# Optimization experiments

Measured on AMD Instinct MI355X. Metric: run time of the kernel, lower is better.

Reference implementation:

```python
import jax, jax.numpy as jnp
import numpy as np

N_CLASSES = 2
N_FEATURES = 10
PSI_DIM = 10


def setup_inputs() -> dict:
    key = jax.random.key(0)
    k1, k2, k3, k4, k5 = jax.random.split(key, 5)
    T = 4_000_000
    x = jax.random.normal(k1, (T, N_FEATURES), dtype=jnp.float32)
    psi_real = jax.random.normal(k2, (PSI_DIM,), dtype=jnp.float32)
    psi_imag = jax.random.normal(k3, (PSI_DIM,), dtype=jnp.float32)
    A_real = jax.random.normal(k4, (N_CLASSES, PSI_DIM, PSI_DIM, N_FEATURES), dtype=jnp.float32)
    A_imag = jax.random.normal(k5, (N_CLASSES, PSI_DIM, PSI_DIM, N_FEATURES), dtype=jnp.float32)
    return {"x": x, "psi_real": psi_real, "psi_imag": psi_imag,
            "A_real": A_real, "A_imag": A_imag}


def _mat(psi1, A, psi2):
    # Batch-independent contraction of the 'i' and 'j' axes: [k, a]
    return jnp.einsum('i,kija,j->ka', psi1, A, psi2)


def reference(x, psi_real, psi_imag, A_real, A_imag):
    x_real = x
    x_imag = jnp.zeros_like(x)
    # Sign pattern from the original 8-term sum:
    #   +rRr -rIr(xi) -iRr(xi) -iIr(xr) -rRi(xr) +rIi(xi) +iRi(xi) +iIi(xr)
    # Coefficient matrix multiplying x_real:
    M_r = (_mat(psi_real, A_real, psi_real)
           - _mat(psi_imag, A_imag, psi_real)
           - _mat(psi_real, A_real, psi_imag)
           + _mat(psi_imag, A_imag, psi_imag))  # [k, a]
    # Coefficient matrix multiplying x_imag:
    M_i = (-_mat(psi_real, A_imag, psi_real)
           - _mat(psi_imag, A_real, psi_real)
           + _mat(psi_real, A_imag, psi_imag)
           + _mat(psi_imag, A_real, psi_imag))  # [k, a]
    # result[t, k] = sum_a x[t, a] * M[k, a]
    return x_real @ M_r.T + x_imag @ M_i.T
```

## Files before the change

### kernel.cpp

```cpp
#include <hip/hip_runtime.h>

constexpr int NC = 2;
constexpr int NF = 10;
constexpr int PD = 10;

__global__ void compute_M_kernel(const float* __restrict__ psi_r,
                                 const float* __restrict__ psi_i,
                                 const float* __restrict__ A_r,
                                 const float* __restrict__ A_i,
                                 float* __restrict__ M) {
    int t = threadIdx.x;
    if (t >= NC * NF) return;
    int k = t / NF;
    int a = t - k * NF;
    float acc = 0.f;
    for (int i = 0; i < PD; ++i) {
        float pri = psi_r[i];
        float pii = psi_i[i];
        for (int j = 0; j < PD; ++j) {
            float dj = psi_r[j] - psi_i[j];
            int idx = ((k * PD + i) * PD + j) * NF + a;
            acc = fmaf(pri * A_r[idx] - pii * A_i[idx], dj, acc);
        }
    }
    M[t] = acc;
}

__global__ __launch_bounds__(256) void apply_M_kernel(
        const float* __restrict__ x, const float* __restrict__ M,
        float* __restrict__ out, int T2) {
    float m0[NF], m1[NF];
#pragma unroll
    for (int a = 0; a < NF; ++a) {
        m0[a] = M[a];
        m1[a] = M[NF + a];
    }
    const int stride = gridDim.x * blockDim.x;
    for (int idx = blockIdx.x * blockDim.x + threadIdx.x; idx < T2; idx += stride) {
        const float4* xp = reinterpret_cast<const float4*>(x + (size_t)idx * 2 * NF);
        float4 v0 = xp[0];
        float4 v1 = xp[1];
        float4 v2 = xp[2];
        float4 v3 = xp[3];
        float4 v4 = xp[4];
        float r0[NF] = {v0.x, v0.y, v0.z, v0.w, v1.x, v1.y, v1.z, v1.w, v2.x, v2.y};
        float r1[NF] = {v2.z, v2.w, v3.x, v3.y, v3.z, v3.w, v4.x, v4.y, v4.z, v4.w};
        float4 o = {0.f, 0.f, 0.f, 0.f};
#pragma unroll
        for (int a = 0; a < NF; ++a) {
            o.x = fmaf(r0[a], m0[a], o.x);
            o.y = fmaf(r0[a], m1[a], o.y);
            o.z = fmaf(r1[a], m0[a], o.z);
            o.w = fmaf(r1[a], m1[a], o.w);
        }
        reinterpret_cast<float4*>(out)[idx] = o;
    }
}

extern "C" void kernel_launch(void* const* d_in, const int* in_sizes, int n_in,
                              void* d_out, int out_size, void* d_ws, size_t ws_size,
                              hipStream_t stream) {
    const float* x     = (const float*)d_in[0];
    const float* psi_r = (const float*)d_in[1];
    const float* psi_i = (const float*)d_in[2];
    const float* A_r   = (const float*)d_in[3];
    const float* A_i   = (const float*)d_in[4];
    float* out = (float*)d_out;
    float* M   = (float*)d_ws;

    const int T  = in_sizes[0] / NF;
    const int T2 = T / 2;

    compute_M_kernel<<<1, 64, 0, stream>>>(psi_r, psi_i, A_r, A_i, M);

    const int threads = 256;
    int blocks = (T2 + threads - 1) / threads;
    if (blocks > 2048) blocks = 2048;
    apply_M_kernel<<<blocks, threads, 0, stream>>>(x, M, out, T2);
}
```

Before: 39.95 us.

## Fuse M computation into apply kernel and stage x via direct global-to-LDS loads

Merges the single-block coefficient kernel into the main kernel, so every block recomputes the 20-entry M matrix in parallel (200 partial sums reduced in shared memory). This removes a kernel launch and the serial dependency between the two launches. The input rows are now loaded as coalesced float4 tiles straight into LDS with global_load_lds, and each thread reads its own 80 bytes back from LDS, instead of issuing strided 80-byte per-thread global loads. In exchange, every block repeats the M work and pays two barriers per tile, and the grid changes to 1792 blocks.

```diff
diff --git a/kernel.cpp b/kernel.cpp
--- a/kernel.cpp
+++ b/kernel.cpp
@@ -4,56 +4,93 @@
 constexpr int NF = 10;
 constexpr int PD = 10;
 
-__global__ void compute_M_kernel(const float* __restrict__ psi_r,
-                                 const float* __restrict__ psi_i,
-                                 const float* __restrict__ A_r,
-                                 const float* __restrict__ A_i,
-                                 float* __restrict__ M) {
-    int t = threadIdx.x;
-    if (t >= NC * NF) return;
-    int k = t / NF;
-    int a = t - k * NF;
-    float acc = 0.f;
-    for (int i = 0; i < PD; ++i) {
-        float pri = psi_r[i];
-        float pii = psi_i[i];
+constexpr int THREADS = 256;
+constexpr int F4_PER_THREAD = 5;
+constexpr int TILE_F4 = THREADS * F4_PER_THREAD;
+constexpr int TILE_FLOATS = TILE_F4 * 4;
+
+__global__ __launch_bounds__(THREADS) void fused_complexnet_kernel(
+        const float* __restrict__ x,
+        const float* __restrict__ psi_r,
+        const float* __restrict__ psi_i,
+        const float* __restrict__ A_r,
+        const float* __restrict__ A_i,
+        float* __restrict__ out,
+        int T2, long totalF4) {
+    __shared__ float Msh[NC * NF];
+    __shared__ float part[NC * NF * PD];
+    __shared__ float tile[TILE_FLOATS];
+
+    const int t = threadIdx.x;
+
+    if (t < NC * NF * PD) {
+        int k = t / (NF * PD);
+        int rem = t - k * (NF * PD);
+        int a = rem / PD;
+        int i = rem - a * PD;
+        float pri = psi_r[i], pii = psi_i[i];
+        float acc = 0.f;
+#pragma unroll
         for (int j = 0; j < PD; ++j) {
             float dj = psi_r[j] - psi_i[j];
             int idx = ((k * PD + i) * PD + j) * NF + a;
             acc = fmaf(pri * A_r[idx] - pii * A_i[idx], dj, acc);
         }
+        part[t] = acc;
     }
-    M[t] = acc;
-}
+    __syncthreads();
+    if (t < NC * NF) {
+        int k = t / NF, a = t - k * NF;
+        float s = 0.f;
+#pragma unroll
+        for (int i = 0; i < PD; ++i) s += part[(k * NF + a) * PD + i];
+        Msh[t] = s;
+    }
+    __syncthreads();
 
-__global__ __launch_bounds__(256) void apply_M_kernel(
-        const float* __restrict__ x, const float* __restrict__ M,
-        float* __restrict__ out, int T2) {
     float m0[NF], m1[NF];
 #pragma unroll
     for (int a = 0; a < NF; ++a) {
-        m0[a] = M[a];
-        m1[a] = M[NF + a];
+        m0[a] = Msh[a];
+        m1[a] = Msh[NF + a];
     }
-    const int stride = gridDim.x * blockDim.x;
-    for (int idx = blockIdx.x * blockDim.x + threadIdx.x; idx < T2; idx += stride) {
-        const float4* xp = reinterpret_cast<const float4*>(x + (size_t)idx * 2 * NF);
-        float4 v0 = xp[0];
-        float4 v1 = xp[1];
-        float4 v2 = xp[2];
-        float4 v3 = xp[3];
-        float4 v4 = xp[4];
-        float r0[NF] = {v0.x, v0.y, v0.z, v0.w, v1.x, v1.y, v1.z, v1.w, v2.x, v2.y};
-        float r1[NF] = {v2.z, v2.w, v3.x, v3.y, v3.z, v3.w, v4.x, v4.y, v4.z, v4.w};
-        float4 o = {0.f, 0.f, 0.f, 0.f};
+
+    const float4* x4 = reinterpret_cast<const float4*>(x);
+    float4* out4 = reinterpret_cast<float4*>(out);
+    const int nTiles = (T2 + THREADS - 1) / THREADS;
+    const int waveBaseF = (t & ~63) * 4;
+
+    for (int tileIdx = blockIdx.x; tileIdx < nTiles; tileIdx += (int)gridDim.x) {
+        const long base4 = (long)tileIdx * TILE_F4;
 #pragma unroll
-        for (int a = 0; a < NF; ++a) {
-            o.x = fmaf(r0[a], m0[a], o.x);
-            o.y = fmaf(r0[a], m1[a], o.y);
-            o.z = fmaf(r1[a], m0[a], o.z);
-            o.w = fmaf(r1[a], m1[a], o.w);
+        for (int q = 0; q < F4_PER_THREAD; ++q) {
+            long g4 = base4 + (long)q * THREADS + t;
+            if (g4 >= totalF4) g4 = totalF4 - 1;
+            const float* ldsdst = &tile[q * (THREADS * 4) + waveBaseF];
+            __builtin_amdgcn_global_load_lds(
+                (const __attribute__((address_space(1))) void*)(x4 + g4),
+                (__attribute__((address_space(3))) void*)ldsdst,
+                16, 0, 0);
         }
-        reinterpret_cast<float4*>(out)[idx] = o;
+        __syncthreads();
+
+        const int rp = tileIdx * THREADS + t;
+        if (rp < T2) {
+            const float4* lp = reinterpret_cast<const float4*>(&tile[t * 20]);
+            float4 v0 = lp[0], v1 = lp[1], v2 = lp[2], v3 = lp[3], v4 = lp[4];
+            float r0[NF] = {v0.x, v0.y, v0.z, v0.w, v1.x, v1.y, v1.z, v1.w, v2.x, v2.y};
+            float r1[NF] = {v2.z, v2.w, v3.x, v3.y, v3.z, v3.w, v4.x, v4.y, v4.z, v4.w};
+            float4 o = {0.f, 0.f, 0.f, 0.f};
+#pragma unroll
+            for (int a = 0; a < NF; ++a) {
+                o.x = fmaf(r0[a], m0[a], o.x);
+                o.y = fmaf(r0[a], m1[a], o.y);
+                o.z = fmaf(r1[a], m0[a], o.z);
+                o.w = fmaf(r1[a], m1[a], o.w);
+            }
+            out4[rp] = o;
+        }
+        __syncthreads();
     }
 }
 
@@ -66,15 +103,14 @@
     const float* A_r   = (const float*)d_in[3];
     const float* A_i   = (const float*)d_in[4];
     float* out = (float*)d_out;
-    float* M   = (float*)d_ws;
 
-    const int T  = in_sizes[0] / NF;
+    const int T = in_sizes[0] / NF;
     const int T2 = T / 2;
+    const long totalF4 = (long)in_sizes[0] / 4;
 
-    compute_M_kernel<<<1, 64, 0, stream>>>(psi_r, psi_i, A_r, A_i, M);
+    const int nTiles = (T2 + THREADS - 1) / THREADS;
+    int blocks = nTiles < 1792 ? nTiles : 1792;
 
-    const int threads = 256;
-    int blocks = (T2 + threads - 1) / threads;
-    if (blocks > 2048) blocks = 2048;
-    apply_M_kernel<<<blocks, threads, 0, stream>>>(x, M, out, T2);
+    fused_complexnet_kernel<<<blocks, THREADS, 0, stream>>>(
+        x, psi_r, psi_i, A_r, A_i, out, T2, totalF4);
 }
```

Measured after the change: 34.34 us. 1.16x faster.

## Fuse M computation into streaming kernel with double-buffered global-to-LDS loads

Applied to the files above, without the earlier changes.

Merges the two kernels into one: every wave recomputes the 2x10 coefficient matrix and broadcasts it with lane shuffles, removing the second launch and the workspace round trip. Each wave then streams 64-row tiles of x straight into LDS with direct global-to-LDS loads, double-buffered and ordered by hand-placed vmcnt waits, and writes a float2 per row. The cost is redundant per-wave recomputation of M, which reads A from global memory, plus reliance on exact vmcnt counting. Rows left over when T is not a multiple of 64 are not processed.

```diff
diff --git a/kernel.cpp b/kernel.cpp
--- a/kernel.cpp
+++ b/kernel.cpp
@@ -4,56 +4,95 @@
 constexpr int NF = 10;
 constexpr int PD = 10;
 
-__global__ void compute_M_kernel(const float* __restrict__ psi_r,
-                                 const float* __restrict__ psi_i,
-                                 const float* __restrict__ A_r,
-                                 const float* __restrict__ A_i,
-                                 float* __restrict__ M) {
-    int t = threadIdx.x;
-    if (t >= NC * NF) return;
-    int k = t / NF;
-    int a = t - k * NF;
+constexpr int THREADS = 256;
+constexpr int NWAVES = THREADS / 64;
+constexpr int TILE_ROWS = 64;
+constexpr int TILE_F4 = TILE_ROWS * NF / 4;
+constexpr int TILE_FLOATS = TILE_ROWS * NF;
+
+__global__ __launch_bounds__(THREADS, 8) void fused_stream_kernel(
+        const float* __restrict__ x,
+        const float* __restrict__ psi_r,
+        const float* __restrict__ psi_i,
+        const float* __restrict__ A_r,
+        const float* __restrict__ A_i,
+        float* __restrict__ out,
+        int nTiles) {
+    __shared__ float tile[NWAVES][2][TILE_FLOATS];
+
+    const int t = threadIdx.x;
+    const int w = t >> 6;
+    const int l = t & 63;
+
     float acc = 0.f;
-    for (int i = 0; i < PD; ++i) {
-        float pri = psi_r[i];
-        float pii = psi_i[i];
-        for (int j = 0; j < PD; ++j) {
-            float dj = psi_r[j] - psi_i[j];
-            int idx = ((k * PD + i) * PD + j) * NF + a;
-            acc = fmaf(pri * A_r[idx] - pii * A_i[idx], dj, acc);
+    if (l < NC * NF) {
+        const int kk = l / NF;
+        const int a = l - kk * NF;
+        for (int i = 0; i < PD; ++i) {
+            float pri = psi_r[i], pii = psi_i[i];
+#pragma unroll
+            for (int j = 0; j < PD; ++j) {
+                float dj = psi_r[j] - psi_i[j];
+                int idx = ((kk * PD + i) * PD + j) * NF + a;
+                acc = fmaf(pri * A_r[idx] - pii * A_i[idx], dj, acc);
+            }
         }
     }
-    M[t] = acc;
-}
-
-__global__ __launch_bounds__(256) void apply_M_kernel(
-        const float* __restrict__ x, const float* __restrict__ M,
-        float* __restrict__ out, int T2) {
     float m0[NF], m1[NF];
 #pragma unroll
     for (int a = 0; a < NF; ++a) {
-        m0[a] = M[a];
-        m1[a] = M[NF + a];
+        m0[a] = __shfl(acc, a);
+        m1[a] = __shfl(acc, NF + a);
     }
-    const int stride = gridDim.x * blockDim.x;
-    for (int idx = blockIdx.x * blockDim.x + threadIdx.x; idx < T2; idx += stride) {
-        const float4* xp = reinterpret_cast<const float4*>(x + (size_t)idx * 2 * NF);
-        float4 v0 = xp[0];
-        float4 v1 = xp[1];
-        float4 v2 = xp[2];
-        float4 v3 = xp[3];
-        float4 v4 = xp[4];
-        float r0[NF] = {v0.x, v0.y, v0.z, v0.w, v1.x, v1.y, v1.z, v1.w, v2.x, v2.y};
-        float r1[NF] = {v2.z, v2.w, v3.x, v3.y, v3.z, v3.w, v4.x, v4.y, v4.z, v4.w};
-        float4 o = {0.f, 0.f, 0.f, 0.f};
+
+    const float4* x4 = reinterpret_cast<const float4*>(x);
+    float2* out2 = reinterpret_cast<float2*>(out);
+    const int W = (int)gridDim.x * NWAVES;
+    const int gw = (int)blockIdx.x * NWAVES + w;
+
+    auto STAGE = [&](int buf, int tk) {
+        const float* dst = &tile[w][buf][0];
+        const float4* src = x4 + (long)tk * TILE_F4;
+        __builtin_amdgcn_global_load_lds(
+            (const __attribute__((address_space(1))) void*)(src + l),
+            (__attribute__((address_space(3))) void*)dst, 16, 0, 0);
+        __builtin_amdgcn_global_load_lds(
+            (const __attribute__((address_space(1))) void*)(src + 64 + l),
+            (__attribute__((address_space(3))) void*)(dst + 256), 16, 0, 0);
+        if (l < 32) {
+            __builtin_amdgcn_global_load_lds(
+                (const __attribute__((address_space(1))) void*)(src + 128 + l),
+                (__attribute__((address_space(3))) void*)(dst + 512), 16, 0, 0);
+        }
+    };
+
+    if (gw >= nTiles) return;
+
+    STAGE(0, gw);
+    int cur = 0;
+    int iter = 0;
+    for (int k = gw; k < nTiles; k += W, ++iter) {
+        const int kn = k + W;
+        const bool hasNext = kn < nTiles;
+        if (hasNext) STAGE(cur ^ 1, kn);
+
+        const int n = (hasNext ? 3 : 0) + (iter ? 1 : 0);
+        if (n == 4)      asm volatile("s_waitcnt vmcnt(4)" ::: "memory");
+        else if (n == 3) asm volatile("s_waitcnt vmcnt(3)" ::: "memory");
+        else if (n == 1) asm volatile("s_waitcnt vmcnt(1)" ::: "memory");
+        else             asm volatile("s_waitcnt vmcnt(0)" ::: "memory");
+
+        const float* row = &tile[w][cur][l * NF];
+        float o0 = 0.f, o1 = 0.f;
 #pragma unroll
         for (int a = 0; a < NF; ++a) {
-            o.x = fmaf(r0[a], m0[a], o.x);
-            o.y = fmaf(r0[a], m1[a], o.y);
-            o.z = fmaf(r1[a], m0[a], o.z);
-            o.w = fmaf(r1[a], m1[a], o.w);
+            float f = row[a];
+            o0 = fmaf(f, m0[a], o0);
+            o1 = fmaf(f, m1[a], o1);
         }
-        reinterpret_cast<float4*>(out)[idx] = o;
+        out2[(long)k * TILE_ROWS + l] = make_float2(o0, o1);
+
+        cur ^= 1;
     }
 }
 
@@ -66,15 +105,13 @@
     const float* A_r   = (const float*)d_in[3];
     const float* A_i   = (const float*)d_in[4];
     float* out = (float*)d_out;
-    float* M   = (float*)d_ws;
 
-    const int T  = in_sizes[0] / NF;
-    const int T2 = T / 2;
+    const int T = in_sizes[0] / NF;
+    const int nTiles = T / TILE_ROWS;
 
-    compute_M_kernel<<<1, 64, 0, stream>>>(psi_r, psi_i, A_r, A_i, M);
+    int blocks = 8 * 256;
+    if (blocks > nTiles / NWAVES + 1) blocks = nTiles / NWAVES + 1;
 
-    const int threads = 256;
-    int blocks = (T2 + threads - 1) / threads;
-    if (blocks > 2048) blocks = 2048;
-    apply_M_kernel<<<blocks, threads, 0, stream>>>(x, M, out, T2);
+    fused_stream_kernel<<<blocks, THREADS, 0, stream>>>(
+        x, psi_r, psi_i, A_r, A_i, out, nTiles);
 }
```

Measured after the change: 42.29 us. 5.9% more time.
